# Performance work log

Hardware: AMD Instinct MI355X
Metric: run time of the kernel (lower is better)

## Reference

```python
import jax, jax.numpy as jnp
import numpy as np

B, S, HID = 1, 2048, 4096
H, KV, D = 32, 8, 128          # query heads, kv heads, head_dim
THETA = 100000.0               # rope base


def setup_inputs() -> dict:
    key = jax.random.key(0)
    k1, k2, k3, k4, k5 = jax.random.split(key, 5)
    hidden_states = jax.random.normal(k1, (B, S, HID), jnp.float32)
    # W_pack: Linear(hidden, H*D + 2*KV*D), torch weight layout [out, in]
    w_pack = jax.random.normal(k2, (H * D + 2 * KV * D, HID), jnp.float32) * 0.02
    w_o = jax.random.normal(k3, (HID, H * D), jnp.float32) * 0.02
    # conv kernels: per-kv-head causal mixing weights of width 2 (softmax-normalized at init)
    conv_k = jax.nn.softmax(jax.random.normal(k4, (KV, 2), jnp.float32), axis=-1)
    conv_v = jax.nn.softmax(jax.random.normal(k5, (KV, 2), jnp.float32), axis=-1)
    return dict(hidden_states=hidden_states, w_pack=w_pack, w_o=w_o,
                conv_k=conv_k, conv_v=conv_v)


def _causal_conv2(u, k):
    """u: [b,s,h,d], k: [h,2]. v[t] = k[h,0]*u[t-1] + k[h,1]*u[t] (zero pad at t=-1).
    Equivalent to custom_convolution with window 2 (unfold+mul+sum)."""
    prev = jnp.pad(u, ((0, 0), (1, 0), (0, 0), (0, 0)))[:, :-1]
    return k[None, None, :, 0:1] * prev + k[None, None, :, 1:2] * u


def _rope(x):
    """Non-interleaved (half-split) rotary over full head_dim. x: [b,s,h,d]."""
    s, d = x.shape[1], x.shape[-1]
    inv = 1.0 / (THETA ** (jnp.arange(0, d, 2, dtype=jnp.float32) / d))
    freqs = jnp.arange(s, dtype=jnp.float32)[:, None] * inv[None, :]  # [s, d/2]
    cos = jnp.cos(freqs)[None, :, None, :]
    sin = jnp.sin(freqs)[None, :, None, :]
    x1, x2 = x[..., : d // 2], x[..., d // 2:]
    return jnp.concatenate([x1 * cos - x2 * sin, x1 * sin + x2 * cos], axis=-1)


def reference(hidden_states, w_pack, w_o, conv_k, conv_v):
    qkv = hidden_states @ w_pack.T                       # [b,s,H*D+2*KV*D]
    q = qkv[..., : H * D].reshape(B, S, H, D)
    k = qkv[..., H * D: H * D + KV * D].reshape(B, S, KV, D)
    v = qkv[..., H * D + KV * D:].reshape(B, S, KV, D)

    # causal depthwise width-2 conv mixing on K and V (prefill path)
    k = _causal_conv2(k, conv_k)
    v = _causal_conv2(v, conv_v)

    # rotary on q, k
    q = _rope(q)
    k = _rope(k)

    # GQA: repeat kv heads to match query heads
    g = H // KV
    k = jnp.repeat(k, g, axis=2)
    v = jnp.repeat(v, g, axis=2)

    scale = 1.0 / np.sqrt(D).astype(np.float32)
    scores = jnp.einsum('bqhd,bkhd->bhqk', q, k) * scale  # [b,H,S,S]
    causal = jnp.tril(jnp.ones((S, S), dtype=bool))
    scores = jnp.where(causal[None, None], scores, jnp.finfo(scores.dtype).min)
    probs = jax.nn.softmax(scores, axis=-1)
    out = jnp.einsum('bhqk,bkhd->bqhd', probs, v).reshape(B, S, H * D)
    return out @ w_o.T
```

## Files before the change

kernel.cpp:

```cpp
#include <hip/hip_runtime.h>
#include <hip/hip_bf16.h>

#define S_LEN 2048
#define HID 4096
#define NH 32
#define NKV 8
#define HD 128

typedef unsigned short u16;
typedef __attribute__((ext_vector_type(4))) float f32x4;
typedef __attribute__((ext_vector_type(8))) short bf16x8;

__device__ __forceinline__ u16 f2bf(float x) {
  union { float f; unsigned u; } c; c.f = x;
  unsigned r = c.u + 0x7FFFu + ((c.u >> 16) & 1u);
  return (u16)(r >> 16);
}

__device__ __forceinline__ float bf2f(u16 x) {
  union { unsigned u; float f; } c; c.u = (unsigned)x << 16;
  return c.f;
}

__device__ __forceinline__ void gload16(const void* g, void* l) {
  __builtin_amdgcn_global_load_lds(
      (const __attribute__((address_space(1))) unsigned int*)g,
      (__attribute__((address_space(3))) unsigned int*)l, 16, 0, 0);
}

__device__ __forceinline__ unsigned cvtpk_bf16(float lo, float hi) {
  unsigned r;
  asm("v_cvt_pk_bf16_f32 %0, %1, %2" : "=v"(r) : "v"(lo), "v"(hi));
  return r;
}

__device__ __forceinline__ float bcastf(float v, int srclane) {
  int r = __builtin_amdgcn_ds_bpermute(srclane << 2, __builtin_bit_cast(int, v));
  return __builtin_bit_cast(float, r);
}

__global__ void prep_kernel(const float* __restrict__ hidden, const float* __restrict__ wpack,
                            const float* __restrict__ wo, u16* __restrict__ hiddenB,
                            u16* __restrict__ wpackB, u16* __restrict__ woB,
                            float2* __restrict__ tab) {
  int bid = blockIdx.x;
  if (bid < 49152) {
    const float* s;
    u16* d;
    int i;
    if (bid < 8192)       { s = hidden; d = hiddenB; i = bid * 256 + threadIdx.x; }
    else if (bid < 32768) { s = wpack;  d = wpackB;  i = (bid - 8192) * 256 + threadIdx.x; }
    else                  { s = wo;     d = woB;     i = (bid - 32768) * 256 + threadIdx.x; }
    float4 v = ((const float4*)s)[i];
    ushort4 o;
    o.x = f2bf(v.x); o.y = f2bf(v.y); o.z = f2bf(v.z); o.w = f2bf(v.w);
    ((ushort4*)d)[i] = o;
  } else {
    int i = (bid - 49152) * 256 + threadIdx.x;
    int t = i >> 6, d = i & 63;
    float inv = expf(-(float)d * (11.512925464970229f / 64.0f));
    float f = (float)t * inv;
    float2 cs; cs.x = cosf(f); cs.y = sinf(f);
    tab[i] = cs;
  }
}

__global__ __launch_bounds__(256) void qkv_pp_kernel(const u16* __restrict__ qkv,
                                                     const float* __restrict__ ck,
                                                     const float* __restrict__ cv,
                                                     const float* __restrict__ tab,
                                                     u16* __restrict__ Q,
                                                     u16* __restrict__ K,
                                                     u16* __restrict__ VT) {
  __shared__ u16 ld[65][128];
  int bid = blockIdx.x;
  if (bid < 4096) {
    int i = bid * 256 + threadIdx.x;
    int d4 = (i & 15) * 4, h = (i >> 4) & 31, t = i >> 9;
    const u16* row = qkv + (size_t)t * 6144 + h * 128;
    ushort4 a = *(const ushort4*)(row + d4);
    ushort4 b = *(const ushort4*)(row + d4 + 64);
    const float4* tf = (const float4*)(tab + ((t << 6) + d4) * 2);
    float4 c01 = tf[0], c23 = tf[1];
    const float SC = 0.12752551286084f;
    float x10 = bf2f(a.x), x11 = bf2f(a.y), x12 = bf2f(a.z), x13 = bf2f(a.w);
    float x20 = bf2f(b.x), x21 = bf2f(b.y), x22 = bf2f(b.z), x23 = bf2f(b.w);
    ushort4 o1, o2;
    o1.x = f2bf((x10 * c01.x - x20 * c01.y) * SC);
    o1.y = f2bf((x11 * c01.z - x21 * c01.w) * SC);
    o1.z = f2bf((x12 * c23.x - x22 * c23.y) * SC);
    o1.w = f2bf((x13 * c23.z - x23 * c23.w) * SC);
    o2.x = f2bf((x10 * c01.y + x20 * c01.x) * SC);
    o2.y = f2bf((x11 * c01.w + x21 * c01.z) * SC);
    o2.z = f2bf((x12 * c23.y + x22 * c23.x) * SC);
    o2.w = f2bf((x13 * c23.w + x23 * c23.z) * SC);
    u16* orow = Q + (((size_t)t * NH + h) << 7);
    *(ushort4*)(orow + d4) = o1;
    *(ushort4*)(orow + d4 + 64) = o2;
  } else if (bid < 5120) {
    int i = (bid - 4096) * 256 + threadIdx.x;
    int d4 = (i & 15) * 4, kv = (i >> 4) & 7, t = i >> 7;
    const u16* cur = qkv + (size_t)t * 6144 + 4096 + kv * 128;
    float c0 = ck[kv * 2], c1 = ck[kv * 2 + 1];
    ushort4 a = *(const ushort4*)(cur + d4);
    ushort4 b = *(const ushort4*)(cur + d4 + 64);
    float x1[4] = { c1 * bf2f(a.x), c1 * bf2f(a.y), c1 * bf2f(a.z), c1 * bf2f(a.w) };
    float x2[4] = { c1 * bf2f(b.x), c1 * bf2f(b.y), c1 * bf2f(b.z), c1 * bf2f(b.w) };
    if (t > 0) {
      const u16* prv = cur - 6144;
      ushort4 pa = *(const ushort4*)(prv + d4);
      ushort4 pb = *(const ushort4*)(prv + d4 + 64);
      x1[0] += c0 * bf2f(pa.x); x1[1] += c0 * bf2f(pa.y); x1[2] += c0 * bf2f(pa.z); x1[3] += c0 * bf2f(pa.w);
      x2[0] += c0 * bf2f(pb.x); x2[1] += c0 * bf2f(pb.y); x2[2] += c0 * bf2f(pb.z); x2[3] += c0 * bf2f(pb.w);
    }
    const float4* tf = (const float4*)(tab + ((t << 6) + d4) * 2);
    float4 c01 = tf[0], c23 = tf[1];
    float cs[4] = { c01.x, c01.z, c23.x, c23.z };
    float sn[4] = { c01.y, c01.w, c23.y, c23.w };
    ushort4 o1, o2;
    o1.x = f2bf(x1[0] * cs[0] - x2[0] * sn[0]);
    o1.y = f2bf(x1[1] * cs[1] - x2[1] * sn[1]);
    o1.z = f2bf(x1[2] * cs[2] - x2[2] * sn[2]);
    o1.w = f2bf(x1[3] * cs[3] - x2[3] * sn[3]);
    o2.x = f2bf(x1[0] * sn[0] + x2[0] * cs[0]);
    o2.y = f2bf(x1[1] * sn[1] + x2[1] * cs[1]);
    o2.z = f2bf(x1[2] * sn[2] + x2[2] * cs[2]);
    o2.w = f2bf(x1[3] * sn[3] + x2[3] * cs[3]);
    u16* orow = K + (((size_t)t * NKV + kv) << 7);
    *(ushort4*)(orow + d4) = o1;
    *(ushort4*)(orow + d4 + 64) = o2;
  } else {
    int sub = bid - 5120;
    int tt = (sub & 31) * 64, kv = sub >> 5;
    float c0 = cv[kv * 2], c1 = cv[kv * 2 + 1];
    for (int idx = threadIdx.x; idx < 65 * 32; idx += 256) {
      int r = idx >> 5, d4 = (idx & 31) * 4;
      int t = tt - 1 + r;
      ushort4 v = (t >= 0) ? *(const ushort4*)(qkv + (size_t)t * 6144 + 5120 + kv * 128 + d4)
                           : (ushort4){0, 0, 0, 0};
      *(ushort4*)(&ld[r][d4]) = v;
    }
    __syncthreads();
    int d = threadIdx.x >> 1, tc = (threadIdx.x & 1) * 32;
    u16* out = VT + ((size_t)kv * 128 + d) * S_LEN + tt + tc;
#pragma unroll
    for (int j = 0; j < 32; ++j)
      out[j] = f2bf(c0 * bf2f(ld[tc + j][d]) + c1 * bf2f(ld[tc + j + 1][d]));
  }
}

#define BM 128
#define BN 128
#define BK 64

template <bool BF16OUT>
__global__ __launch_bounds__(256, 2) void gemm_nt_kernel(const u16* __restrict__ A,
                                                         const u16* __restrict__ B,
                                                         void* __restrict__ C,
                                                         int M, int N, int K) {
  __shared__ __align__(16) u16 lA[BM * BK];
  __shared__ __align__(16) u16 lB[BN * BK];
  const int tid = threadIdx.x;
  const int wid = tid >> 6, lane = tid & 63;
  const int bm = blockIdx.y * BM, bn = blockIdx.x * BN;
  const int wr = (wid >> 1) * 64, wc = (wid & 1) * 64;
  const int lr = lane & 15, lg = lane >> 4;
  f32x4 acc[4][4] = {};
  const char* Ab = (const char*)A;
  const char* Bb = (const char*)B;
  const int nk = K / BK;
  for (int kt = 0; kt < nk; ++kt) {
    const size_t k0b = (size_t)kt * (BK * 2);
    __syncthreads();
#pragma unroll
    for (int i = 0; i < 4; ++i) {
      int off = (i * 4 + wid) * 1024 + lane * 16;
      int row = off >> 7, inrow = off & 127;
      int sw = inrow ^ ((row & 7) << 4);
      gload16(Ab + (size_t)(bm + row) * (K * 2) + k0b + sw, (char*)lA + (i * 4 + wid) * 1024);
      gload16(Bb + (size_t)(bn + row) * (K * 2) + k0b + sw, (char*)lB + (i * 4 + wid) * 1024);
    }
    __syncthreads();
    bf16x8 af[4][2], bfv[4][2];
#pragma unroll
    for (int m = 0; m < 4; ++m)
#pragma unroll
      for (int ks = 0; ks < 2; ++ks) {
        int row = wr + m * 16 + lr;
        int boff = row * 128 + ((ks * 64 + lg * 16) ^ ((row & 7) << 4));
        af[m][ks] = *(const bf16x8*)((const char*)lA + boff);
      }
#pragma unroll
    for (int n = 0; n < 4; ++n)
#pragma unroll
      for (int ks = 0; ks < 2; ++ks) {
        int row = wc + n * 16 + lr;
        int boff = row * 128 + ((ks * 64 + lg * 16) ^ ((row & 7) << 4));
        bfv[n][ks] = *(const bf16x8*)((const char*)lB + boff);
      }
#pragma unroll
    for (int m = 0; m < 4; ++m)
#pragma unroll
      for (int n = 0; n < 4; ++n)
#pragma unroll
        for (int ks = 0; ks < 2; ++ks)
          acc[m][n] = __builtin_amdgcn_mfma_f32_16x16x32_bf16(af[m][ks], bfv[n][ks], acc[m][n], 0, 0, 0);
  }
#pragma unroll
  for (int m = 0; m < 4; ++m)
#pragma unroll
    for (int n = 0; n < 4; ++n)
#pragma unroll
      for (int r = 0; r < 4; ++r) {
        int row = bm + wr + m * 16 + lg * 4 + r;
        int col = bn + wc + n * 16 + lr;
        if (BF16OUT)
          ((u16*)C)[(size_t)row * N + col] = f2bf(acc[m][n][r]);
        else
          ((float*)C)[(size_t)row * N + col] = acc[m][n][r];
      }
}

__global__ __launch_bounds__(256, 2) void attn_kernel(const u16* __restrict__ Q,
                                                      const u16* __restrict__ K,
                                                      const u16* __restrict__ VT,
                                                      u16* __restrict__ O) {
  __shared__ __align__(16) u16 lK[2][64 * 128];
  __shared__ __align__(16) u16 lV[2][128 * 64];
  __shared__ __align__(16) u16 lP[4][2][16 * 64];
  const int tid = threadIdx.x;
  const int wid = tid >> 6, lane = tid & 63;
  const int lr = lane & 15, lg = lane >> 4;
  const int g = blockIdx.x;
  const int s = g & 255;
  const int h = s >> 3, j = s & 7;
  const int b = (g < 256) ? (15 - j) : j;
  const int kvh = h >> 2;
  const int qtA = 2 * b, qtB = 2 * b + 1;
  const int qrowA = qtA * 64 + wid * 16 + lr;
  const int qrowB = qtB * 64 + wid * 16 + lr;

  bf16x8 qfA[4], qfB[4];
#pragma unroll
  for (int ks = 0; ks < 4; ++ks) {
    qfA[ks] = *(const bf16x8*)(Q + (((size_t)qrowA * NH + h) << 7) + ks * 32 + lg * 8);
    qfB[ks] = *(const bf16x8*)(Q + (((size_t)qrowB * NH + h) << 7) + ks * 32 + lg * 8);
  }

  f32x4 oA[8] = {}, oB[8] = {};
  float mA = -1e30f, sumA = 0.f, mB = -1e30f, sumB = 0.f;

  const char* Kb = (const char*)K;
  const char* Vb = (const char*)VT;
  char* pbA = (char*)lP[wid][0];
  char* pbB = (char*)lP[wid][1];

  auto stage = [&](int buf, int kt) {
    char* dK = (char*)lK[buf];
    char* dV = (char*)lV[buf];
#pragma unroll
    for (int i = 0; i < 4; ++i) {
      int off = (i * 4 + wid) * 1024 + lane * 16;
      int t = off >> 8, inrow = off & 255;
      gload16(Kb + (((size_t)((kt * 64 + t) * NKV + kvh)) << 8) + (inrow ^ ((t & 7) << 4)),
              dK + (i * 4 + wid) * 1024);
      int d = off >> 7, inr2 = off & 127;
      gload16(Vb + ((size_t)(kvh * 128 + d)) * (S_LEN * 2) + kt * 128 + (inr2 ^ ((d & 7) << 4)),
              dV + (i * 4 + wid) * 1024);
    }
  };

  auto smx = [&](f32x4* sv, float& mm, float& ll, f32x4* o, char* pbuf, bool diag, int qrow, int kt) {
    if (diag) {
#pragma unroll
      for (int n = 0; n < 4; ++n)
#pragma unroll
        for (int r = 0; r < 4; ++r) {
          int kg = kt * 64 + n * 16 + lg * 4 + r;
          if (kg > qrow) sv[n][r] = -1e30f;
        }
    }
    float pm = sv[0][0];
#pragma unroll
    for (int n = 0; n < 4; ++n)
#pragma unroll
      for (int r = 0; r < 4; ++r) pm = fmaxf(pm, sv[n][r]);
    pm = fmaxf(pm, __shfl_xor(pm, 16));
    pm = fmaxf(pm, __shfl_xor(pm, 32));
    if (__any(pm > mm + 8.f)) {
      float mn = fmaxf(mm, pm);
      float al = exp2f(mm - mn);
      mm = mn;
      ll *= al;
      float alo[4];
#pragma unroll
      for (int r = 0; r < 4; ++r) alo[r] = bcastf(al, lg * 4 + r);
#pragma unroll
      for (int nt = 0; nt < 8; ++nt)
#pragma unroll
        for (int r = 0; r < 4; ++r) o[nt][r] *= alo[r];
    }
    float rs = 0.f;
#pragma unroll
    for (int n = 0; n < 4; ++n)
#pragma unroll
      for (int r = 0; r < 4; ++r) {
        float p = exp2f(sv[n][r] - mm);
        sv[n][r] = p;
        rs += p;
      }
    rs += __shfl_xor(rs, 16);
    rs += __shfl_xor(rs, 32);
    ll += rs;
#pragma unroll
    for (int n = 0; n < 4; ++n) {
      uint2 w;
      w.x = cvtpk_bf16(sv[n][0], sv[n][1]);
      w.y = cvtpk_bf16(sv[n][2], sv[n][3]);
      *(uint2*)(pbuf + ((lr * 128 + n * 32 + lg * 8) ^ ((lr & 7) << 4))) = w;
    }
  };

  stage(0, 0);
  __syncthreads();
  for (int kt = 0; kt <= qtB; ++kt) {
    int cur = kt & 1;
    if (kt < qtB) stage(cur ^ 1, kt + 1);
    const char* kb = (const char*)lK[cur];
    const char* vb = (const char*)lV[cur];
    const bool doA = (kt <= qtA);

    f32x4 svA[4], svB[4];
#pragma unroll
    for (int n = 0; n < 4; ++n) {
      f32x4 aA = {}, aB = {};
#pragma unroll
      for (int ks = 0; ks < 4; ++ks) {
        int trow = n * 16 + lr;
        int boff = trow * 256 + ((ks * 64 + lg * 16) ^ ((trow & 7) << 4));
        bf16x8 kf = *(const bf16x8*)(kb + boff);
        aB = __builtin_amdgcn_mfma_f32_16x16x32_bf16(kf, qfB[ks], aB, 0, 0, 0);
        aA = __builtin_amdgcn_mfma_f32_16x16x32_bf16(kf, qfA[ks], aA, 0, 0, 0);
      }
      svA[n] = aA; svB[n] = aB;
    }

    if (doA) smx(svA, mA, sumA, oA, pbA, kt == qtA, qrowA, kt);
    smx(svB, mB, sumB, oB, pbB, kt == qtB, qrowB, kt);

#pragma unroll
    for (int ks = 0; ks < 2; ++ks) {
      int poff = (lr * 128 + 64 * ks + 16 * lg) ^ ((lr & 7) << 4);
      bf16x8 pfB = *(const bf16x8*)(pbB + poff);
      bf16x8 pfA = *(const bf16x8*)(pbA + poff);
#pragma unroll
      for (int nt = 0; nt < 8; ++nt) {
        int drow = nt * 16 + lr;
        int vboff = drow * 128 + ((ks * 64 + lg * 16) ^ ((drow & 7) << 4));
        bf16x8 vf = *(const bf16x8*)(vb + vboff);
        oB[nt] = __builtin_amdgcn_mfma_f32_16x16x32_bf16(pfB, vf, oB[nt], 0, 0, 0);
        if (doA) oA[nt] = __builtin_amdgcn_mfma_f32_16x16x32_bf16(pfA, vf, oA[nt], 0, 0, 0);
      }
    }
    __syncthreads();
  }

  float riA = 1.0f / sumA, riB = 1.0f / sumB;
  float rA[4], rB[4];
#pragma unroll
  for (int r = 0; r < 4; ++r) {
    rA[r] = bcastf(riA, lg * 4 + r);
    rB[r] = bcastf(riB, lg * 4 + r);
  }
#pragma unroll
  for (int nt = 0; nt < 8; ++nt)
#pragma unroll
    for (int r = 0; r < 4; ++r) {
      int rowA = qtA * 64 + wid * 16 + lg * 4 + r;
      int rowB = qtB * 64 + wid * 16 + lg * 4 + r;
      int col = nt * 16 + lr;
      O[(size_t)rowA * 4096 + h * 128 + col] = f2bf(oA[nt][r] * rA[r]);
      O[(size_t)rowB * 4096 + h * 128 + col] = f2bf(oB[nt][r] * rB[r]);
    }
}

extern "C" void kernel_launch(void* const* d_in, const int* in_sizes, int n_in,
                              void* d_out, int out_size, void* d_ws, size_t ws_size,
                              hipStream_t stream) {
  const float* hidden = (const float*)d_in[0];
  const float* wpack  = (const float*)d_in[1];
  const float* wo     = (const float*)d_in[2];
  const float* convk  = (const float*)d_in[3];
  const float* convv  = (const float*)d_in[4];
  float* out = (float*)d_out;

  char* w = (char*)d_ws;
  u16*  hiddenB = (u16*)w;
  u16*  wpackB  = (u16*)(w + 16777216);
  u16*  qkvB    = (u16*)(w + 67108864);
  u16*  qrope   = (u16*)(w + 92274688);
  u16*  krope   = (u16*)(w + 109051904);
  u16*  vT      = (u16*)(w + 113246208);
  float* tab    = (float*)(w + 117440512);
  u16*  woB     = (u16*)(w + 118489088);

  prep_kernel<<<49664, 256, 0, stream>>>(hidden, wpack, wo, hiddenB, wpackB, woB, (float2*)tab);
  gemm_nt_kernel<true><<<dim3(48, 16), 256, 0, stream>>>(hiddenB, wpackB, qkvB, 2048, 6144, 4096);
  qkv_pp_kernel<<<5376, 256, 0, stream>>>(qkvB, convk, convv, tab, qrope, krope, vT);
  attn_kernel<<<512, 256, 0, stream>>>(qrope, krope, vT, hiddenB);
  gemm_nt_kernel<false><<<dim3(32, 16), 256, 0, stream>>>(hiddenB, woB, out, 2048, 4096, 4096);
}
```

Before: 485.9 us.

## Read V directly from global in attention and move wo conversion to postprocess

The attention kernel stops staging V tiles through LDS. Each lane now loads its V fragments straight from global memory (transposed VT) inside the PV loop, which frees LDS so occupancy can be raised to 3 blocks per CU. Separately, the fp32-to-bf16 conversion of w_o moves from the prep kernel into extra blocks of the qkv postprocess kernel. The tradeoff is that the direct global V loads are uncached and sit on the MFMA critical path, so latency may be exposed.

New measurement: 582.2 us. 19.8% more time.

```diff
diff --git a/kernel.cpp b/kernel.cpp
--- a/kernel.cpp
+++ b/kernel.cpp
@@ -40,23 +40,21 @@
 }
 
 __global__ void prep_kernel(const float* __restrict__ hidden, const float* __restrict__ wpack,
-                            const float* __restrict__ wo, u16* __restrict__ hiddenB,
-                            u16* __restrict__ wpackB, u16* __restrict__ woB,
+                            u16* __restrict__ hiddenB, u16* __restrict__ wpackB,
                             float2* __restrict__ tab) {
   int bid = blockIdx.x;
-  if (bid < 49152) {
+  if (bid < 32768) {
     const float* s;
     u16* d;
     int i;
-    if (bid < 8192)       { s = hidden; d = hiddenB; i = bid * 256 + threadIdx.x; }
-    else if (bid < 32768) { s = wpack;  d = wpackB;  i = (bid - 8192) * 256 + threadIdx.x; }
-    else                  { s = wo;     d = woB;     i = (bid - 32768) * 256 + threadIdx.x; }
+    if (bid < 8192) { s = hidden; d = hiddenB; i = bid * 256 + threadIdx.x; }
+    else            { s = wpack;  d = wpackB;  i = (bid - 8192) * 256 + threadIdx.x; }
     float4 v = ((const float4*)s)[i];
     ushort4 o;
     o.x = f2bf(v.x); o.y = f2bf(v.y); o.z = f2bf(v.z); o.w = f2bf(v.w);
     ((ushort4*)d)[i] = o;
   } else {
-    int i = (bid - 49152) * 256 + threadIdx.x;
+    int i = (bid - 32768) * 256 + threadIdx.x;
     int t = i >> 6, d = i & 63;
     float inv = expf(-(float)d * (11.512925464970229f / 64.0f));
     float f = (float)t * inv;
@@ -69,9 +67,11 @@
                                                      const float* __restrict__ ck,
                                                      const float* __restrict__ cv,
                                                      const float* __restrict__ tab,
+                                                     const float* __restrict__ wo,
                                                      u16* __restrict__ Q,
                                                      u16* __restrict__ K,
-                                                     u16* __restrict__ VT) {
+                                                     u16* __restrict__ VT,
+                                                     u16* __restrict__ woB) {
   __shared__ u16 ld[65][128];
   int bid = blockIdx.x;
   if (bid < 4096) {
@@ -129,7 +129,7 @@
     u16* orow = K + (((size_t)t * NKV + kv) << 7);
     *(ushort4*)(orow + d4) = o1;
     *(ushort4*)(orow + d4 + 64) = o2;
-  } else {
+  } else if (bid < 5376) {
     int sub = bid - 5120;
     int tt = (sub & 31) * 64, kv = sub >> 5;
     float c0 = cv[kv * 2], c1 = cv[kv * 2 + 1];
@@ -146,6 +146,12 @@
 #pragma unroll
     for (int j = 0; j < 32; ++j)
       out[j] = f2bf(c0 * bf2f(ld[tc + j][d]) + c1 * bf2f(ld[tc + j + 1][d]));
+  } else {
+    int i = (bid - 5376) * 256 + threadIdx.x;
+    float4 v = ((const float4*)wo)[i];
+    ushort4 o;
+    o.x = f2bf(v.x); o.y = f2bf(v.y); o.z = f2bf(v.z); o.w = f2bf(v.w);
+    ((ushort4*)woB)[i] = o;
   }
 }
 
@@ -221,12 +227,11 @@
       }
 }
 
-__global__ __launch_bounds__(256, 2) void attn_kernel(const u16* __restrict__ Q,
+__global__ __launch_bounds__(256, 3) void attn_kernel(const u16* __restrict__ Q,
                                                       const u16* __restrict__ K,
                                                       const u16* __restrict__ VT,
                                                       u16* __restrict__ O) {
   __shared__ __align__(16) u16 lK[2][64 * 128];
-  __shared__ __align__(16) u16 lV[2][128 * 64];
   __shared__ __align__(16) u16 lP[4][2][16 * 64];
   const int tid = threadIdx.x;
   const int wid = tid >> 6, lane = tid & 63;
@@ -251,22 +256,18 @@
   float mA = -1e30f, sumA = 0.f, mB = -1e30f, sumB = 0.f;
 
   const char* Kb = (const char*)K;
-  const char* Vb = (const char*)VT;
+  const u16* Vrow = VT + (size_t)(kvh * 128 + lr) * S_LEN + lg * 8;
   char* pbA = (char*)lP[wid][0];
   char* pbB = (char*)lP[wid][1];
 
   auto stage = [&](int buf, int kt) {
     char* dK = (char*)lK[buf];
-    char* dV = (char*)lV[buf];
 #pragma unroll
     for (int i = 0; i < 4; ++i) {
       int off = (i * 4 + wid) * 1024 + lane * 16;
       int t = off >> 8, inrow = off & 255;
       gload16(Kb + (((size_t)((kt * 64 + t) * NKV + kvh)) << 8) + (inrow ^ ((t & 7) << 4)),
               dK + (i * 4 + wid) * 1024);
-      int d = off >> 7, inr2 = off & 127;
-      gload16(Vb + ((size_t)(kvh * 128 + d)) * (S_LEN * 2) + kt * 128 + (inr2 ^ ((d & 7) << 4)),
-              dV + (i * 4 + wid) * 1024);
     }
   };
 
@@ -327,7 +328,6 @@
     int cur = kt & 1;
     if (kt < qtB) stage(cur ^ 1, kt + 1);
     const char* kb = (const char*)lK[cur];
-    const char* vb = (const char*)lV[cur];
     const bool doA = (kt <= qtA);
 
     f32x4 svA[4], svB[4];
@@ -348,6 +348,7 @@
     if (doA) smx(svA, mA, sumA, oA, pbA, kt == qtA, qrowA, kt);
     smx(svB, mB, sumB, oB, pbB, kt == qtB, qrowB, kt);
 
+    const u16* vbase = Vrow + kt * 64;
 #pragma unroll
     for (int ks = 0; ks < 2; ++ks) {
       int poff = (lr * 128 + 64 * ks + 16 * lg) ^ ((lr & 7) << 4);
@@ -355,9 +356,7 @@
       bf16x8 pfA = *(const bf16x8*)(pbA + poff);
 #pragma unroll
       for (int nt = 0; nt < 8; ++nt) {
-        int drow = nt * 16 + lr;
-        int vboff = drow * 128 + ((ks * 64 + lg * 16) ^ ((drow & 7) << 4));
-        bf16x8 vf = *(const bf16x8*)(vb + vboff);
+        bf16x8 vf = *(const bf16x8*)(vbase + (size_t)(nt * 16) * S_LEN + ks * 32);
         oB[nt] = __builtin_amdgcn_mfma_f32_16x16x32_bf16(pfB, vf, oB[nt], 0, 0, 0);
         if (doA) oA[nt] = __builtin_amdgcn_mfma_f32_16x16x32_bf16(pfA, vf, oA[nt], 0, 0, 0);
       }
@@ -404,9 +403,9 @@
   float* tab    = (float*)(w + 117440512);
   u16*  woB     = (u16*)(w + 118489088);
 
-  prep_kernel<<<49664, 256, 0, stream>>>(hidden, wpack, wo, hiddenB, wpackB, woB, (float2*)tab);
+  prep_kernel<<<33280, 256, 0, stream>>>(hidden, wpack, hiddenB, wpackB, (float2*)tab);
   gemm_nt_kernel<true><<<dim3(48, 16), 256, 0, stream>>>(hiddenB, wpackB, qkvB, 2048, 6144, 4096);
-  qkv_pp_kernel<<<5376, 256, 0, stream>>>(qkvB, convk, convv, tab, qrope, krope, vT);
+  qkv_pp_kernel<<<21760, 256, 0, stream>>>(qkvB, convk, convv, tab, wo, qrope, krope, vT, woB);
   attn_kernel<<<512, 256, 0, stream>>>(qrope, krope, vT, hiddenB);
   gemm_nt_kernel<false><<<dim3(32, 16), 256, 0, stream>>>(hiddenB, woB, out, 2048, 4096, 4096);
 }
```
